# Performance work log

Measured on AMD Instinct MI355X. Metric: run time of the kernel, lower is better.

Reference implementation:

```python
import jax, jax.numpy as jnp
import numpy as np
from jax import lax

VOCAB, E, HD = 50000, 128, 256
H = HD // 2            # per-direction LSTM hidden
K = 9                  # tagset size
START, STOP = 7, 8
B, T = 64, 1024
NEG = -10000.0


def setup_inputs() -> dict:
    key = jax.random.key(0)
    ks = jax.random.split(key, 14)
    s = 0.1
    sentence = jax.random.randint(ks[0], (B, T), 0, VOCAB)
    embed = jax.random.normal(ks[1], (VOCAB, E), jnp.float32) * s
    w_ih_f = jax.random.normal(ks[2], (4 * H, E), jnp.float32) * s
    w_hh_f = jax.random.normal(ks[3], (4 * H, H), jnp.float32) * s
    b_ih_f = jax.random.normal(ks[4], (4 * H,), jnp.float32) * s
    b_hh_f = jax.random.normal(ks[5], (4 * H,), jnp.float32) * s
    w_ih_b = jax.random.normal(ks[6], (4 * H, E), jnp.float32) * s
    w_hh_b = jax.random.normal(ks[7], (4 * H, H), jnp.float32) * s
    b_ih_b = jax.random.normal(ks[8], (4 * H,), jnp.float32) * s
    b_hh_b = jax.random.normal(ks[9], (4 * H,), jnp.float32) * s
    w_out = jax.random.normal(ks[10], (K, HD), jnp.float32) * s
    b_out = jax.random.normal(ks[11], (K,), jnp.float32) * s
    transitions = jax.random.normal(ks[12], (K, K), jnp.float32)
    transitions = transitions.at[START, :].set(NEG).at[:, STOP].set(NEG)
    return dict(sentence=sentence, embed=embed,
                w_ih_f=w_ih_f, w_hh_f=w_hh_f, b_ih_f=b_ih_f, b_hh_f=b_hh_f,
                w_ih_b=w_ih_b, w_hh_b=w_hh_b, b_ih_b=b_ih_b, b_hh_b=b_hh_b,
                w_out=w_out, b_out=b_out, transitions=transitions)


def _lstm_dir(x_tbe, w_ih, w_hh, b_ih, b_hh):
    # x_tbe: [T, B, E] -> hidden states [T, B, H]; zero initial state
    # (original passes no hidden to self.lstm, so PyTorch uses zeros)
    bsz = x_tbe.shape[1]
    def step(carry, x_t):
        h, c = carry
        gates = x_t @ w_ih.T + b_ih + h @ w_hh.T + b_hh   # [B, 4H]
        i, f, g, o = jnp.split(gates, 4, axis=-1)          # torch gate order
        i, f, o = jax.nn.sigmoid(i), jax.nn.sigmoid(f), jax.nn.sigmoid(o)
        g = jnp.tanh(g)
        c = f * c + i * g
        h = o * jnp.tanh(c)
        return (h, c), h
    init = (jnp.zeros((bsz, H), x_tbe.dtype), jnp.zeros((bsz, H), x_tbe.dtype))
    _, hs = lax.scan(step, init, x_tbe)
    return hs


def _features(sentence, embed, w_ih_f, w_hh_f, b_ih_f, b_hh_f,
              w_ih_b, w_hh_b, b_ih_b, b_hh_b, w_out, b_out):
    x = embed[sentence]                      # [B, T, E]
    x_tbe = jnp.transpose(x, (1, 0, 2))      # [T, B, E]
    h_f = _lstm_dir(x_tbe, w_ih_f, w_hh_f, b_ih_f, b_hh_f)
    h_b = _lstm_dir(x_tbe[::-1], w_ih_b, w_hh_b, b_ih_b, b_hh_b)[::-1]
    h = jnp.concatenate([h_f, h_b], axis=-1)  # [T, B, 2H]
    feats = h @ w_out.T + b_out               # [T, B, K]
    return feats


def _viterbi(feats_tbk, transitions):
    # feats_tbk: [T, B, K]. Batched version of _viterbi_decode.
    bsz = feats_tbk.shape[1]
    init = jnp.full((K,), NEG, feats_tbk.dtype).at[START].set(0.0)
    delta0 = jnp.broadcast_to(init, (bsz, K))
    def step(delta, feat_t):
        # scores[b, next, prev] = delta[b, prev] + trans[next, prev]
        scores = delta[:, None, :] + transitions[None, :, :]
        bp = jnp.argmax(scores, axis=-1)                 # [B, K]
        delta = jnp.max(scores, axis=-1) + feat_t        # [B, K]
        return delta, bp
    delta, bps = lax.scan(step, delta0, feats_tbk)       # bps: [T, B, K]
    terminal = delta + transitions[STOP][None, :]
    best_last = jnp.argmax(terminal, axis=-1)            # [B]
    score = jnp.max(terminal, axis=-1)                   # [B]
    def back(tag, bp_t):
        prev = jnp.take_along_axis(bp_t, tag[:, None], axis=1)[:, 0]
        return prev, prev
    _, path_rev = lax.scan(back, best_last, bps[::-1])   # [T, B]
    # path_rev reversed = [START, tag_0, ..., tag_{T-2}] -> drop START, add last
    path = jnp.concatenate([path_rev[::-1][1:], best_last[None, :]], axis=0)
    return score, jnp.transpose(path, (1, 0))            # [B], [B, T]


def reference(sentence, embed, w_ih_f, w_hh_f, b_ih_f, b_hh_f,
              w_ih_b, w_hh_b, b_ih_b, b_hh_b, w_out, b_out, transitions):
    feats = _features(sentence, embed, w_ih_f, w_hh_f, b_ih_f, b_hh_f,
                      w_ih_b, w_hh_b, b_ih_b, b_hh_b, w_out, b_out)
    score, tag_seq = _viterbi(feats, transitions)
    return score, tag_seq
```

## Files before the change

### kernel.cpp

```cpp
#include <hip/hip_runtime.h>
#include <hip/hip_bf16.h>

#define Tn 1024
#define Bn 64
#define En 128
#define G4 512
#define NEGV -10000.0f

typedef short bh8 __attribute__((ext_vector_type(8)));
typedef float fl4 __attribute__((ext_vector_type(4)));
typedef int i8v __attribute__((ext_vector_type(8)));

#if __has_builtin(__builtin_amdgcn_exp2f)
#define EXP2(x) __builtin_amdgcn_exp2f(x)
#else
#define EXP2(x) exp2f(x)
#endif
#if __has_builtin(__builtin_amdgcn_rcpf)
#define RCP(x) __builtin_amdgcn_rcpf(x)
#else
#define RCP(x) (1.0f / (x))
#endif

#define LOG2E  1.4426950408889634f
#define LOG2E2 2.8853900817779268f

__device__ __forceinline__ float bf2f(unsigned short u) {
    unsigned int v = ((unsigned int)u) << 16;
    float f;
    __builtin_memcpy(&f, &v, 4);
    return f;
}
__device__ __forceinline__ unsigned short f2bf(float f) {
    unsigned int u;
    __builtin_memcpy(&u, &f, 4);
    u = (u + 0x7fffu + ((u >> 16) & 1u)) >> 16;
    return (unsigned short)u;
}
__device__ __forceinline__ unsigned cvt_pk_bf16(float lo, float hi) {
    unsigned r;
    asm("v_cvt_pk_bf16_f32 %0, %1, %2" : "=v"(r) : "v"(lo), "v"(hi));
    return r;
}
__device__ __forceinline__ unsigned short f2bf_hw(float x) {
    return (unsigned short)(cvt_pk_bf16(x, 0.0f) & 0xffffu);
}
__device__ __forceinline__ float asf(unsigned int u) {
    float f;
    __builtin_memcpy(&f, &u, 4);
    return f;
}
__device__ __forceinline__ float i2f(int u) {
    float f;
    __builtin_memcpy(&f, &u, 4);
    return f;
}
__device__ __forceinline__ int f2i(float f) {
    int u;
    __builtin_memcpy(&u, &f, 4);
    return u;
}

__device__ __forceinline__ unsigned char f8enc(float x) {
#if __has_builtin(__builtin_amdgcn_cvt_pk_fp8_f32)
    int pk = __builtin_amdgcn_cvt_pk_fp8_f32(x, 0.0f, 0, false);
    return (unsigned char)(pk & 0xff);
#else
    unsigned u;
    __builtin_memcpy(&u, &x, 4);
    unsigned s = (u >> 31) << 7;
    float a = fabsf(x);
    if (!(a > 0.0f)) return (unsigned char)s;
    if (a >= 464.0f) return (unsigned char)(s | 0x7E);
    if (a < 0.015625f) {
        int q = (int)rintf(a * 512.0f);
        return (unsigned char)(s | (unsigned)q);
    }
    int ex;
    (void)frexpf(a, &ex);
    int E = ex - 1;
    float t = ldexpf(a, -E);
    int m3 = (int)rintf((t - 1.0f) * 8.0f);
    if (m3 == 8) { m3 = 0; E += 1; }
    if (E > 8) return (unsigned char)(s | 0x7E);
    return (unsigned char)(s | ((unsigned)(E + 7) << 3) | (unsigned)m3);
#endif
}

__device__ __forceinline__ void barrier_lds_only() {
    __builtin_amdgcn_s_waitcnt(0xC07F);
    __builtin_amdgcn_s_barrier();
}

__global__ __launch_bounds__(256) void k_wcvt(
    const float* __restrict__ wf, const float* __restrict__ wb,
    unsigned char* __restrict__ o)
{
    const int i = blockIdx.x * 256 + threadIdx.x;
    const float v = (i < 65536) ? wf[i] : wb[i - 65536];
    o[i] = f8enc(v * 64.0f);
}

__global__ __launch_bounds__(256) void k_inproj(
    const int* __restrict__ sent, const float* __restrict__ embed,
    const float* __restrict__ w_ih_f, const float* __restrict__ b_ih_f, const float* __restrict__ b_hh_f,
    const float* __restrict__ w_ih_b, const float* __restrict__ b_ih_b, const float* __restrict__ b_hh_b,
    unsigned short* __restrict__ G_f, unsigned short* __restrict__ G_b)
{
    __shared__ unsigned short Asm[128][136];
    __shared__ unsigned short Bsm[128][136];
    const int tid = threadIdx.x;
    const int dir = blockIdx.z;
    const float* w_ih = dir ? w_ih_b : w_ih_f;
    const float* bi   = dir ? b_ih_b : b_ih_f;
    const float* bh   = dir ? b_hh_b : b_hh_f;
    unsigned short* Gout = dir ? G_b : G_f;

    const int mt = blockIdx.x, nt = blockIdx.y;
    const int r0 = mt * 128, n0 = nt * 128;

    const int srow = tid >> 1;
    const int ch = (tid & 1) * 64;
    {
        const int rg = r0 + srow;
        const int tt = rg >> 6, bb = rg & 63;
        const int tok = sent[bb * Tn + tt];
        const int np = n0 + srow;
        const int norig = ((np & 3) << 7) + (np >> 2);
        const float* ar = embed + (size_t)tok * En + ch;
        const float* br = w_ih + (size_t)norig * En + ch;
#pragma unroll
        for (int i = 0; i < 64; i += 4) {
            float4 v = *(const float4*)(ar + i);
            *(unsigned*)&Asm[srow][ch + i]     = cvt_pk_bf16(v.x, v.y);
            *(unsigned*)&Asm[srow][ch + i + 2] = cvt_pk_bf16(v.z, v.w);
            float4 u = *(const float4*)(br + i);
            *(unsigned*)&Bsm[srow][ch + i]     = cvt_pk_bf16(u.x, u.y);
            *(unsigned*)&Bsm[srow][ch + i + 2] = cvt_pk_bf16(u.z, u.w);
        }
    }
    __syncthreads();

    const int w = tid >> 6, lane = tid & 63;
    const int ln = lane & 15, lq = lane >> 4;
    const int nwb = w * 32;

    fl4 acc[8][2];
#pragma unroll
    for (int mi = 0; mi < 8; ++mi)
#pragma unroll
        for (int ni = 0; ni < 2; ++ni) acc[mi][ni] = (fl4){0.f, 0.f, 0.f, 0.f};

#pragma unroll
    for (int kt = 0; kt < 4; ++kt) {
        const int kc = kt * 32 + lq * 8;
        bh8 a[8], bf[2];
#pragma unroll
        for (int mi = 0; mi < 8; ++mi) a[mi] = *(const bh8*)&Asm[mi * 16 + ln][kc];
#pragma unroll
        for (int ni = 0; ni < 2; ++ni) bf[ni] = *(const bh8*)&Bsm[nwb + ni * 16 + ln][kc];
#pragma unroll
        for (int mi = 0; mi < 8; ++mi)
#pragma unroll
            for (int ni = 0; ni < 2; ++ni)
                acc[mi][ni] = __builtin_amdgcn_mfma_f32_16x16x32_bf16(a[mi], bf[ni], acc[mi][ni], 0, 0, 0);
    }

    float bias[2], gsc[2];
#pragma unroll
    for (int ni = 0; ni < 2; ++ni) {
        const int np = n0 + nwb + ni * 16 + ln;
        const int norig = ((np & 3) << 7) + (np >> 2);
        bias[ni] = bi[norig] + bh[norig];
        gsc[ni] = ((np & 3) == 2) ? LOG2E2 : LOG2E;
    }
#pragma unroll
    for (int mi = 0; mi < 8; ++mi)
#pragma unroll
        for (int ni = 0; ni < 2; ++ni) {
            const int np = n0 + nwb + ni * 16 + ln;
#pragma unroll
            for (int rg = 0; rg < 4; ++rg) {
                const int m = mi * 16 + lq * 4 + rg;
                const size_t r = (size_t)(r0 + m);
                Gout[(r << 9) + np] = f2bf_hw((acc[mi][ni][rg] + bias[ni]) * gsc[ni]);
            }
        }
}

__global__ __launch_bounds__(512, 2) void k_lstm(
    const unsigned char* __restrict__ whh8,
    const unsigned short* __restrict__ G_f, const unsigned short* __restrict__ G_b,
    unsigned short* __restrict__ h_f, unsigned short* __restrict__ h_b)
{
    const int tid = threadIdx.x;
    const int w = tid >> 6;
    const int lane = tid & 63;
    const int ln = lane & 15;
    const int quad = lane >> 4;
    const int b = blockIdx.x;
    const int dir = blockIdx.y;
    const unsigned short* Gd = dir ? G_b : G_f;
    unsigned short* ho = dir ? h_b : h_f;

    const int j = w * 16 + ln;

    __shared__ __align__(16) unsigned char hls8[2][128];

    const unsigned char* wb8 = whh8 + (size_t)dir * 65536 + quad * 32;
    const i8v w0 = *(const i8v*)(wb8 + ((size_t)(0 * 128 + j) << 7));
    const i8v w1 = *(const i8v*)(wb8 + ((size_t)(1 * 128 + j) << 7));
    const i8v w2 = *(const i8v*)(wb8 + ((size_t)(2 * 128 + j) << 7));
    const i8v w3 = *(const i8v*)(wb8 + ((size_t)(3 * 128 + j) << 7));

    if (tid < 64) ((unsigned*)hls8)[tid] = 0u;
    float c = 0.0f;
    __syncthreads();

    uint2 gp[4];
#pragma unroll
    for (int u = 0; u < 4; ++u) {
        const int tt = dir ? (Tn - 1 - u) : u;
        gp[u] = *(const uint2*)(Gd + (((size_t)tt * Bn + b) << 9) + (j << 2));
    }

    const float dsL  = 0.0009765625f * LOG2E;
    const float ds2L = 0.0009765625f * LOG2E2;

    const float cds = (quad == 2) ? ds2L : -dsL;
    const unsigned gsign = (quad == 2) ? 0u : 0x80000000u;
    const int gshift = (quad & 1) ? 0 : 16;
    const int bp0 = (0 * 16 + ln) << 2;
    const int bp1 = (1 * 16 + ln) << 2;
    const int bp2 = (2 * 16 + ln) << 2;
    const int bp3 = (3 * 16 + ln) << 2;

    for (int blk = 0; blk < Tn / 4; ++blk) {
#pragma unroll
        for (int u = 0; u < 4; ++u) {
            const int s = blk * 4 + u;
            const int t = dir ? (Tn - 1 - s) : s;
            const int p = u & 1;

            const uint2 gv = gp[u];

            if (s + 4 < Tn) {
                const int tt = dir ? (Tn - 5 - s) : (s + 4);
                gp[u] = *(const uint2*)(Gd + (((size_t)tt * Bn + b) << 9) + (j << 2));
            }

            const i8v ha = *(const i8v*)&hls8[p][quad * 32];

            const fl4 z = (fl4){0.f, 0.f, 0.f, 0.f};
            fl4 a0 = __builtin_amdgcn_mfma_scale_f32_16x16x128_f8f6f4(
                         ha, w0, z, 0, 0, 0, 0x7F7F7F7F, 0, 0x7F7F7F7F);
            fl4 a1 = __builtin_amdgcn_mfma_scale_f32_16x16x128_f8f6f4(
                         ha, w1, z, 0, 0, 0, 0x7F7F7F7F, 0, 0x7F7F7F7F);
            fl4 a2 = __builtin_amdgcn_mfma_scale_f32_16x16x128_f8f6f4(
                         ha, w2, z, 0, 0, 0, 0x7F7F7F7F, 0, 0x7F7F7F7F);
            fl4 a3 = __builtin_amdgcn_mfma_scale_f32_16x16x128_f8f6f4(
                         ha, w3, z, 0, 0, 0, 0x7F7F7F7F, 0, 0x7F7F7F7F);

            float a01 = (quad & 1) ? a1[0] : a0[0];
            float a23 = (quad & 1) ? a3[0] : a2[0];
            float aown = (quad & 2) ? a23 : a01;
            unsigned wsel = (quad & 2) ? gv.y : gv.x;
            unsigned gb = ((wsel << gshift) & 0xffff0000u) ^ gsign;
            float pre = __builtin_fmaf(aown, cds, asf(gb));
            float tq = RCP(1.0f + EXP2(pre));
            int tqi = f2i(tq);
            float iv = i2f(__builtin_amdgcn_ds_bpermute(bp0, tqi));
            float fv = i2f(__builtin_amdgcn_ds_bpermute(bp1, tqi));
            float tg = i2f(__builtin_amdgcn_ds_bpermute(bp2, tqi));
            float ov = i2f(__builtin_amdgcn_ds_bpermute(bp3, tqi));
            float gvv = __builtin_fmaf(-2.0f, tg, 1.0f);
            c = __builtin_fmaf(fv, c, iv * gvv);
            float r2 = RCP(1.0f + EXP2(c * LOG2E2));
            float hn = ov * __builtin_fmaf(-2.0f, r2, 1.0f);

            if (quad == 0) {
                hls8[1 - p][j] = f8enc(hn * 16.0f);
                ho[(((size_t)t * Bn + b) << 7) + j] = f2bf(hn);
            }

            barrier_lds_only();
        }
    }
}

__global__ __launch_bounds__(256) void k_feats(
    const unsigned short* __restrict__ h_f, const unsigned short* __restrict__ h_b,
    const float* __restrict__ w_out, const float* __restrict__ b_out,
    float* __restrict__ feats)
{
    __shared__ float wl[256][12];
    __shared__ float bl[12];
    const int tid = threadIdx.x;
#pragma unroll
    for (int s = 0; s < 9; ++s) wl[tid][s] = w_out[s * 256 + tid];
#pragma unroll
    for (int s = 9; s < 12; ++s) wl[tid][s] = 0.0f;
    if (tid < 12) bl[tid] = (tid < 9) ? b_out[tid] : 0.0f;
    __syncthreads();

    const int r = blockIdx.x * 256 + tid;
    const unsigned short* hfr = h_f + (size_t)r * 128;
    const unsigned short* hbr = h_b + (size_t)r * 128;
    float acc[12];
#pragma unroll
    for (int k = 0; k < 12; ++k) acc[k] = bl[k];

    for (int ch = 0; ch < 32; ++ch) {
        const unsigned short* src = (ch < 16) ? (hfr + ch * 8) : (hbr + (ch - 16) * 8);
        uint4 hv = *(const uint4*)src;
        unsigned int hw0 = hv.x, hw1 = hv.y, hw2 = hv.z, hw3 = hv.w;
        const int jb = ch * 8;
#pragma unroll
        for (int q = 0; q < 8; ++q) {
            unsigned int word = (q < 2) ? hw0 : ((q < 4) ? hw1 : ((q < 6) ? hw2 : hw3));
            unsigned short hs = (q & 1) ? (unsigned short)(word >> 16) : (unsigned short)(word & 0xffff);
            float hf = bf2f(hs);
            const float* wrp = &wl[jb + q][0];
            float4 w0 = *(const float4*)(wrp);
            float4 w1 = *(const float4*)(wrp + 4);
            float4 w2 = *(const float4*)(wrp + 8);
            acc[0] += hf * w0.x; acc[1] += hf * w0.y; acc[2] += hf * w0.z; acc[3] += hf * w0.w;
            acc[4] += hf * w1.x; acc[5] += hf * w1.y; acc[6] += hf * w1.z; acc[7] += hf * w1.w;
            acc[8] += hf * w2.x; acc[9] += hf * w2.y; acc[10] += hf * w2.z; acc[11] += hf * w2.w;
        }
    }
    const int t = r >> 6, b = r & 63;
    float* fr = feats + (size_t)b * 9216 + (size_t)t * 9;
#pragma unroll
    for (int k = 0; k < 9; ++k) fr[k] = acc[k];
}

__global__ __launch_bounds__(64) void k_viterbi(
    const float* __restrict__ feats, const float* __restrict__ trans,
    float* __restrict__ out)
{
    __shared__ __align__(16) unsigned char bp[1024 * 16];
    __shared__ __align__(16) float fl[1024 * 9];
    __shared__ unsigned char pt[1024];

    const int b = blockIdx.x, tid = threadIdx.x;

    {
        const float4* fsrc = (const float4*)(feats + (size_t)b * 9216);
        float4* fdst = (float4*)fl;
        for (int i = tid; i < 2304; i += 64) fdst[i] = fsrc[i];
    }

    const int n9 = (tid < 9) ? tid : 8;
    float trn[9];
#pragma unroll
    for (int p = 0; p < 9; ++p) trn[p] = trans[n9 * 9 + p];
    float trs = (tid < 9) ? trans[8 * 9 + tid] : -3.0e38f;

    float delta = (n9 == 7) ? 0.0f : NEGV;
    __syncthreads();

    float fnext = fl[n9];
    for (int t = 0; t < 1024; ++t) {
        float d0 = __shfl(delta, 0, 64);
        float d1 = __shfl(delta, 1, 64);
        float d2 = __shfl(delta, 2, 64);
        float d3 = __shfl(delta, 3, 64);
        float d4 = __shfl(delta, 4, 64);
        float d5 = __shfl(delta, 5, 64);
        float d6 = __shfl(delta, 6, 64);
        float d7 = __shfl(delta, 7, 64);
        float d8 = __shfl(delta, 8, 64);
        float fhere = fnext;
        if (t < 1023) fnext = fl[(t + 1) * 9 + n9];

        float s0 = d0 + trn[0], s1 = d1 + trn[1], s2 = d2 + trn[2];
        float s3 = d3 + trn[3], s4 = d4 + trn[4], s5 = d5 + trn[5];
        float s6 = d6 + trn[6], s7 = d7 + trn[7], s8 = d8 + trn[8];

        float m012 = fmaxf(fmaxf(s0, s1), s2);
        float m345 = fmaxf(fmaxf(s3, s4), s5);
        float m678 = fmaxf(fmaxf(s6, s7), s8);
        float m = fmaxf(fmaxf(m012, m345), m678);
        delta = m + fhere;

        float v01 = (s1 > s0) ? s1 : s0; int a01 = (s1 > s0) ? 1 : 0;
        float v23 = (s3 > s2) ? s3 : s2; int a23 = (s3 > s2) ? 3 : 2;
        float v45 = (s5 > s4) ? s5 : s4; int a45 = (s5 > s4) ? 5 : 4;
        float v67 = (s7 > s6) ? s7 : s6; int a67 = (s7 > s6) ? 7 : 6;
        float v03 = (v23 > v01) ? v23 : v01; int a03 = (v23 > v01) ? a23 : a01;
        float v47 = (v67 > v45) ? v67 : v45; int a47 = (v67 > v45) ? a67 : a45;
        float v07 = (v47 > v03) ? v47 : v03; int a07 = (v47 > v03) ? a47 : a03;
        int am = (s8 > v07) ? 8 : a07;

        if (tid < 9) bp[t * 16 + tid] = (unsigned char)am;
    }

    float tv = (tid < 9) ? (delta + trs) : -3.0e38f;
    int bi = tid;
#pragma unroll
    for (int off = 8; off >= 1; off >>= 1) {
        float ov = __shfl_down(tv, off, 64);
        int oi = __shfl_down(bi, off, 64);
        if (ov > tv || (ov == tv && oi < bi)) { tv = ov; bi = oi; }
    }
    int best = __shfl(bi, 0, 64);
    if (tid == 0) out[b] = tv;

    if (tid == 0) {
        int tag = best;
        for (int t0 = 1023; t0 >= 0; t0 -= 8) {
            uint4 rows[8];
#pragma unroll
            for (int i = 0; i < 8; ++i) rows[i] = *(const uint4*)&bp[(t0 - i) * 16];
#pragma unroll
            for (int i = 0; i < 8; ++i) {
                pt[t0 - i] = (unsigned char)tag;
                uint4 rw = rows[i];
                unsigned int sel = (unsigned int)tag >> 2;
                unsigned int word = (sel == 0) ? rw.x : ((sel == 1) ? rw.y : rw.z);
                tag = (int)((word >> ((tag & 3) * 8)) & 0xffu);
            }
        }
    }
    for (int i = tid; i < 1024; i += 64) {
        out[64 + b * 1024 + i] = (float)pt[i];
    }
}

extern "C" void kernel_launch(void* const* d_in, const int* in_sizes, int n_in,
                              void* d_out, int out_size, void* d_ws, size_t ws_size,
                              hipStream_t stream) {
    const int*   sent   = (const int*)d_in[0];
    const float* embed  = (const float*)d_in[1];
    const float* w_ih_f = (const float*)d_in[2];
    const float* w_hh_f = (const float*)d_in[3];
    const float* b_ih_f = (const float*)d_in[4];
    const float* b_hh_f = (const float*)d_in[5];
    const float* w_ih_b = (const float*)d_in[6];
    const float* w_hh_b = (const float*)d_in[7];
    const float* b_ih_b = (const float*)d_in[8];
    const float* b_hh_b = (const float*)d_in[9];
    const float* w_out  = (const float*)d_in[10];
    const float* b_out  = (const float*)d_in[11];
    const float* trans  = (const float*)d_in[12];
    float* out = (float*)d_out;

    unsigned short* G_f = (unsigned short*)d_ws;
    unsigned short* G_b = G_f + (size_t)Tn * Bn * G4;
    unsigned short* h_f = G_b + (size_t)Tn * Bn * G4;
    unsigned short* h_b = h_f + (size_t)Tn * Bn * 128;
    float* feats = (float*)(h_b + (size_t)Tn * Bn * 128);
    unsigned char* whh8 = (unsigned char*)(feats + (size_t)Tn * Bn * 9);

    k_wcvt<<<512, 256, 0, stream>>>(w_hh_f, w_hh_b, whh8);
    k_inproj<<<dim3(512, 4, 2), 256, 0, stream>>>(sent, embed,
        w_ih_f, b_ih_f, b_hh_f, w_ih_b, b_ih_b, b_hh_b, G_f, G_b);
    k_lstm<<<dim3(64, 2), 512, 0, stream>>>(whh8, G_f, G_b, h_f, h_b);
    k_feats<<<256, 256, 0, stream>>>(h_f, h_b, w_out, b_out, feats);
    k_viterbi<<<64, 64, 0, stream>>>(feats, trans, out);
}
```

Baseline: 779.9 us.

## Reuse embedding tile across all gate tiles and pre-convert input weights

The input-projection kernel now loads and converts each 128-row embedding tile once and loops over all 8 (direction, gate-tile) weight chunks, double-buffering the pre-permuted bf16 weight tiles in LDS. The weight permutation and bf16 conversion move into the existing weight-convert kernel, so the projection reads ready-made bf16 tiles. This removes the 8x redundant gathered embedding loads and the per-block fp32 weight conversion. In exchange there are 8x fewer, longer-running blocks (512 vs 4096), more LDS per block, which may lower occupancy, and a barrier per chunk.

```diff
diff --git a/kernel.cpp b/kernel.cpp
--- a/kernel.cpp
+++ b/kernel.cpp
@@ -94,98 +94,124 @@
 
 __global__ __launch_bounds__(256) void k_wcvt(
     const float* __restrict__ wf, const float* __restrict__ wb,
-    unsigned char* __restrict__ o)
+    const float* __restrict__ wih_f, const float* __restrict__ wih_b,
+    unsigned char* __restrict__ o, unsigned short* __restrict__ wihP)
 {
     const int i = blockIdx.x * 256 + threadIdx.x;
-    const float v = (i < 65536) ? wf[i] : wb[i - 65536];
-    o[i] = f8enc(v * 64.0f);
+    if (i < 131072) {
+        const float v = (i < 65536) ? wf[i] : wb[i - 65536];
+        o[i] = f8enc(v * 64.0f);
+    } else {
+        const int j = i - 131072;
+        const int dir = j >> 16;
+        const int np = (j >> 7) & 511;
+        const int k = j & 127;
+        const int norig = ((np & 3) << 7) + (np >> 2);
+        const float* w = dir ? wih_b : wih_f;
+        wihP[j] = f2bf_hw(w[norig * 128 + k]);
+    }
 }
 
 __global__ __launch_bounds__(256) void k_inproj(
     const int* __restrict__ sent, const float* __restrict__ embed,
-    const float* __restrict__ w_ih_f, const float* __restrict__ b_ih_f, const float* __restrict__ b_hh_f,
-    const float* __restrict__ w_ih_b, const float* __restrict__ b_ih_b, const float* __restrict__ b_hh_b,
+    const unsigned short* __restrict__ wihP,
+    const float* __restrict__ b_ih_f, const float* __restrict__ b_hh_f,
+    const float* __restrict__ b_ih_b, const float* __restrict__ b_hh_b,
     unsigned short* __restrict__ G_f, unsigned short* __restrict__ G_b)
 {
     __shared__ unsigned short Asm[128][136];
-    __shared__ unsigned short Bsm[128][136];
+    __shared__ unsigned short Bsm[2][128][136];
     const int tid = threadIdx.x;
-    const int dir = blockIdx.z;
-    const float* w_ih = dir ? w_ih_b : w_ih_f;
-    const float* bi   = dir ? b_ih_b : b_ih_f;
-    const float* bh   = dir ? b_hh_b : b_hh_f;
-    unsigned short* Gout = dir ? G_b : G_f;
-
-    const int mt = blockIdx.x, nt = blockIdx.y;
-    const int r0 = mt * 128, n0 = nt * 128;
-
-    const int srow = tid >> 1;
-    const int ch = (tid & 1) * 64;
+    const int mt = blockIdx.x;
+    const int r0 = mt * 128;
+
     {
+        const int srow = tid >> 1;
+        const int ch = (tid & 1) * 64;
         const int rg = r0 + srow;
         const int tt = rg >> 6, bb = rg & 63;
         const int tok = sent[bb * Tn + tt];
-        const int np = n0 + srow;
-        const int norig = ((np & 3) << 7) + (np >> 2);
         const float* ar = embed + (size_t)tok * En + ch;
-        const float* br = w_ih + (size_t)norig * En + ch;
 #pragma unroll
         for (int i = 0; i < 64; i += 4) {
             float4 v = *(const float4*)(ar + i);
             *(unsigned*)&Asm[srow][ch + i]     = cvt_pk_bf16(v.x, v.y);
             *(unsigned*)&Asm[srow][ch + i + 2] = cvt_pk_bf16(v.z, v.w);
-            float4 u = *(const float4*)(br + i);
-            *(unsigned*)&Bsm[srow][ch + i]     = cvt_pk_bf16(u.x, u.y);
-            *(unsigned*)&Bsm[srow][ch + i + 2] = cvt_pk_bf16(u.z, u.w);
-        }
-    }
+        }
+    }
+
+    const int brow = tid >> 1;
+    const int bhalf = (tid & 1) * 64;
+#define STAGE_B(cidx)                                                          \
+    {                                                                          \
+        const int d_ = (cidx) >> 2, nt_ = (cidx) & 3, pb_ = (cidx) & 1;        \
+        const uint4* s4 = (const uint4*)(wihP + ((size_t)d_ << 16) +           \
+                          (size_t)(nt_ * 128 + brow) * 128 + bhalf);           \
+        uint4* d4 = (uint4*)&Bsm[pb_][brow][bhalf];                            \
+        _Pragma("unroll")                                                      \
+        for (int ii = 0; ii < 8; ++ii) d4[ii] = s4[ii];                        \
+    }
+
+    STAGE_B(0);
     __syncthreads();
 
     const int w = tid >> 6, lane = tid & 63;
     const int ln = lane & 15, lq = lane >> 4;
     const int nwb = w * 32;
 
-    fl4 acc[8][2];
-#pragma unroll
-    for (int mi = 0; mi < 8; ++mi)
-#pragma unroll
-        for (int ni = 0; ni < 2; ++ni) acc[mi][ni] = (fl4){0.f, 0.f, 0.f, 0.f};
-
-#pragma unroll
-    for (int kt = 0; kt < 4; ++kt) {
-        const int kc = kt * 32 + lq * 8;
-        bh8 a[8], bf[2];
-#pragma unroll
-        for (int mi = 0; mi < 8; ++mi) a[mi] = *(const bh8*)&Asm[mi * 16 + ln][kc];
-#pragma unroll
-        for (int ni = 0; ni < 2; ++ni) bf[ni] = *(const bh8*)&Bsm[nwb + ni * 16 + ln][kc];
+    for (int cidx = 0; cidx < 8; ++cidx) {
+        if (cidx + 1 < 8) STAGE_B(cidx + 1);
+        const int dir = cidx >> 2, nt = cidx & 3, pb = cidx & 1;
+
+        fl4 acc[8][2];
 #pragma unroll
         for (int mi = 0; mi < 8; ++mi)
 #pragma unroll
-            for (int ni = 0; ni < 2; ++ni)
-                acc[mi][ni] = __builtin_amdgcn_mfma_f32_16x16x32_bf16(a[mi], bf[ni], acc[mi][ni], 0, 0, 0);
-    }
-
-    float bias[2], gsc[2];
-#pragma unroll
-    for (int ni = 0; ni < 2; ++ni) {
-        const int np = n0 + nwb + ni * 16 + ln;
-        const int norig = ((np & 3) << 7) + (np >> 2);
-        bias[ni] = bi[norig] + bh[norig];
-        gsc[ni] = ((np & 3) == 2) ? LOG2E2 : LOG2E;
-    }
-#pragma unroll
-    for (int mi = 0; mi < 8; ++mi)
+            for (int ni = 0; ni < 2; ++ni) acc[mi][ni] = (fl4){0.f, 0.f, 0.f, 0.f};
+
+#pragma unroll
+        for (int kt = 0; kt < 4; ++kt) {
+            const int kc = kt * 32 + lq * 8;
+            bh8 a[8], bf[2];
+#pragma unroll
+            for (int mi = 0; mi < 8; ++mi) a[mi] = *(const bh8*)&Asm[mi * 16 + ln][kc];
+#pragma unroll
+            for (int ni = 0; ni < 2; ++ni) bf[ni] = *(const bh8*)&Bsm[pb][nwb + ni * 16 + ln][kc];
+#pragma unroll
+            for (int mi = 0; mi < 8; ++mi)
+#pragma unroll
+                for (int ni = 0; ni < 2; ++ni)
+                    acc[mi][ni] = __builtin_amdgcn_mfma_f32_16x16x32_bf16(a[mi], bf[ni], acc[mi][ni], 0, 0, 0);
+        }
+
+        const float* bi = dir ? b_ih_b : b_ih_f;
+        const float* bh = dir ? b_hh_b : b_hh_f;
+        unsigned short* Gout = dir ? G_b : G_f;
+
+        float bias[2], gsc[2];
 #pragma unroll
         for (int ni = 0; ni < 2; ++ni) {
-            const int np = n0 + nwb + ni * 16 + ln;
-#pragma unroll
-            for (int rg = 0; rg < 4; ++rg) {
-                const int m = mi * 16 + lq * 4 + rg;
-                const size_t r = (size_t)(r0 + m);
-                Gout[(r << 9) + np] = f2bf_hw((acc[mi][ni][rg] + bias[ni]) * gsc[ni]);
+            const int np = nt * 128 + nwb + ni * 16 + ln;
+            const int norig = ((np & 3) << 7) + (np >> 2);
+            bias[ni] = bi[norig] + bh[norig];
+            gsc[ni] = ((np & 3) == 2) ? LOG2E2 : LOG2E;
+        }
+#pragma unroll
+        for (int mi = 0; mi < 8; ++mi)
+#pragma unroll
+            for (int ni = 0; ni < 2; ++ni) {
+                const int np = nt * 128 + nwb + ni * 16 + ln;
+#pragma unroll
+                for (int rg = 0; rg < 4; ++rg) {
+                    const int m = mi * 16 + lq * 4 + rg;
+                    const size_t r = (size_t)(r0 + m);
+                    Gout[(r << 9) + np] = f2bf_hw((acc[mi][ni][rg] + bias[ni]) * gsc[ni]);
+                }
             }
-        }
+
+        __syncthreads();
+    }
+#undef STAGE_B
 }
 
 __global__ __launch_bounds__(512, 2) void k_lstm(
@@ -452,10 +478,11 @@
     unsigned short* h_b = h_f + (size_t)Tn * Bn * 128;
     float* feats = (float*)(h_b + (size_t)Tn * Bn * 128);
     unsigned char* whh8 = (unsigned char*)(feats + (size_t)Tn * Bn * 9);
-
-    k_wcvt<<<512, 256, 0, stream>>>(w_hh_f, w_hh_b, whh8);
-    k_inproj<<<dim3(512, 4, 2), 256, 0, stream>>>(sent, embed,
-        w_ih_f, b_ih_f, b_hh_f, w_ih_b, b_ih_b, b_hh_b, G_f, G_b);
+    unsigned short* wihP = (unsigned short*)(whh8 + 131072);
+
+    k_wcvt<<<1024, 256, 0, stream>>>(w_hh_f, w_hh_b, w_ih_f, w_ih_b, whh8, wihP);
+    k_inproj<<<512, 256, 0, stream>>>(sent, embed, wihP,
+        b_ih_f, b_hh_f, b_ih_b, b_hh_b, G_f, G_b);
     k_lstm<<<dim3(64, 2), 512, 0, stream>>>(whh8, G_f, G_b, h_f, h_b);
     k_feats<<<256, 256, 0, stream>>>(h_f, h_b, w_out, b_out, feats);
     k_viterbi<<<64, 64, 0, stream>>>(feats, trans, out);
```

After: 737.8 us. -5.4%, faster.
